# Performance work log

Hardware: AMD Instinct MI355X
Metric: run time of the kernel (lower is better)

The kernel has to match this reference:

```python
import jax, jax.numpy as jnp
import numpy as np


def setup_inputs() -> dict:
    key = jax.random.key(0)
    k1, k2 = jax.random.split(key)
    pred_pts = jax.random.normal(k1, (8, 3, 4096), dtype=jnp.float32)  # [B,3,N]
    gt_pts = jax.random.normal(k2, (8, 4096, 3), dtype=jnp.float32)    # [B,M,3]
    return {"pred_pts": pred_pts, "gt_pts": gt_pts}


def _chamfer(p, g):
    # p: [B,N,3], g: [B,M,3]
    # squared euclidean distance matrix via ||p||^2 + ||g||^2 - 2 p.g
    pn = jnp.sum(p * p, axis=-1)  # [B,N]
    gn = jnp.sum(g * g, axis=-1)  # [B,M]
    cross = jnp.einsum("bnd,bmd->bnm", p, g)  # [B,N,M]
    D = pn[:, :, None] + gn[:, None, :] - 2.0 * cross  # [B,N,M]
    dist1 = jnp.min(D, axis=2)  # [B,N] min over gt for each pred point
    dist2 = jnp.min(D, axis=1)  # [B,M] min over pred for each gt point
    return dist1, dist2


def reference(pred_pts, gt_pts):
    p = jnp.swapaxes(pred_pts, -2, -1).astype(jnp.float32)  # [B,N,3]
    g = gt_pts  # [B,M,3]
    dist1, dist2 = _chamfer(p, g)
    per_batch = jnp.mean(dist1, axis=1) + jnp.mean(dist2, axis=1)  # [B]
    loss = jnp.sum(per_batch) / gt_pts.shape[0]
    return loss
```

## Files before the change

kernel.cpp:

```cpp
#include <hip/hip_runtime.h>

#define NPTS 4096
#define BATCH 8
#define BLK 256
#define P 4
#define CHUNK 256
#define REPS 2
#define NSLOT 8
#define OWN_PER_BLK (BLK * P)
#define OWN_BLKS (NPTS / OWN_PER_BLK)
#define BLOCKS_PER_PASS (BATCH * OWN_BLKS * NSLOT)
#define TOTAL_BLOCKS (2 * BLOCKS_PER_PASS)
#define HALF_OWN (BATCH * NPTS)
#define TOTAL_OWN (2 * HALF_OWN)
#define COMBINE_BLOCKS (TOTAL_OWN / BLK)

__global__ __launch_bounds__(BLK, 2) void chamfer_partial_kernel(
    const float* __restrict__ pred,
    const float* __restrict__ gt,
    float* __restrict__ partial)
{
    __shared__ float4 s[CHUNK];

    const int bid  = blockIdx.x;
    const int pass = bid / BLOCKS_PER_PASS;
    int r = bid - pass * BLOCKS_PER_PASS;
    const int c = r % NSLOT;
    r /= NSLOT;
    const int b = r / OWN_BLKS;
    const int j = r - b * OWN_BLKS;
    const int t = threadIdx.x;

    const float* p = pred + (size_t)b * 3 * NPTS;
    const float* g = gt   + (size_t)b * NPTS * 3;

    float x[P], y[P], z[P];
    #pragma unroll
    for (int k = 0; k < P; ++k) {
        int idx = j * OWN_PER_BLK + k * BLK + t;
        if (pass == 0) { x[k] = p[idx]; y[k] = p[NPTS + idx]; z[k] = p[2 * NPTS + idx]; }
        else           { x[k] = g[idx * 3 + 0]; y[k] = g[idx * 3 + 1]; z[k] = g[idx * 3 + 2]; }
    }

    float qx, qy, qz;
    {
        int i = (c * REPS) * CHUNK + t;
        if (pass == 0) { qx = g[i * 3 + 0]; qy = g[i * 3 + 1]; qz = g[i * 3 + 2]; }
        else           { qx = p[i]; qy = p[NPTS + i]; qz = p[2 * NPTS + i]; }
    }

    float acc[P];
    #pragma unroll
    for (int k = 0; k < P; ++k) acc[k] = 3.4e38f;

    #pragma unroll
    for (int rep = 0; rep < REPS; ++rep) {
        __syncthreads();
        s[t] = make_float4(-2.f * qx, -2.f * qy, -2.f * qz,
                           fmaf(qx, qx, fmaf(qy, qy, qz * qz)));
        __syncthreads();

        if (rep + 1 < REPS) {
            int i = (c * REPS + rep + 1) * CHUNK + t;
            if (pass == 0) { qx = g[i * 3 + 0]; qy = g[i * 3 + 1]; qz = g[i * 3 + 2]; }
            else           { qx = p[i]; qy = p[NPTS + i]; qz = p[2 * NPTS + i]; }
        }

        #pragma unroll 2
        for (int ss = 0; ss < CHUNK; ss += 2) {
            float4 q0 = s[ss + 0];
            float4 q1 = s[ss + 1];
            #pragma unroll
            for (int k = 0; k < P; ++k) {
                float d0 = fmaf(x[k], q0.x, fmaf(y[k], q0.y, fmaf(z[k], q0.z, q0.w)));
                float d1 = fmaf(x[k], q1.x, fmaf(y[k], q1.y, fmaf(z[k], q1.z, q1.w)));
                acc[k] = fminf(fminf(d0, d1), acc[k]);
            }
        }
    }

    #pragma unroll
    for (int k = 0; k < P; ++k) {
        int idx = j * OWN_PER_BLK + k * BLK + t;
        int o = pass * HALF_OWN + b * NPTS + idx;
        float n2 = fmaf(x[k], x[k], fmaf(y[k], y[k], z[k] * z[k]));
        partial[(size_t)c * TOTAL_OWN + o] = n2 + acc[k];
    }
}

__global__ __launch_bounds__(BLK) void chamfer_combine_kernel(
    const float* __restrict__ partial, float* __restrict__ bsum)
{
    __shared__ float red[BLK / 64];
    const int t = threadIdx.x;
    const int o = blockIdx.x * BLK + t;
    float v = 3.4e38f;
    #pragma unroll
    for (int cc = 0; cc < NSLOT; ++cc)
        v = fminf(v, partial[(size_t)cc * TOTAL_OWN + o]);
    #pragma unroll
    for (int off = 32; off > 0; off >>= 1)
        v += __shfl_down(v, off, 64);
    if ((t & 63) == 0) red[t >> 6] = v;
    __syncthreads();
    if (t == 0) bsum[blockIdx.x] = red[0] + red[1] + red[2] + red[3];
}

__global__ __launch_bounds__(COMBINE_BLOCKS) void chamfer_final_kernel(
    const float* __restrict__ bsum, float* __restrict__ out)
{
    __shared__ float red[COMBINE_BLOCKS / 64];
    const int t = threadIdx.x;
    float v = bsum[t];
    #pragma unroll
    for (int off = 32; off > 0; off >>= 1)
        v += __shfl_down(v, off, 64);
    if ((t & 63) == 0) red[t >> 6] = v;
    __syncthreads();
    if (t == 0) {
        float s = 0.f;
        #pragma unroll
        for (int w = 0; w < COMBINE_BLOCKS / 64; ++w) s += red[w];
        out[0] = s * (1.0f / ((float)NPTS * (float)BATCH));
    }
}

extern "C" void kernel_launch(void* const* d_in, const int* in_sizes, int n_in,
                              void* d_out, int out_size, void* d_ws, size_t ws_size,
                              hipStream_t stream) {
    const float* pred = (const float*)d_in[0];
    const float* gt   = (const float*)d_in[1];
    float* out = (float*)d_out;

    float* partial = (float*)d_ws;
    float* bsum    = partial + (size_t)NSLOT * TOTAL_OWN;

    chamfer_partial_kernel<<<TOTAL_BLOCKS, BLK, 0, stream>>>(pred, gt, partial);
    chamfer_combine_kernel<<<COMBINE_BLOCKS, BLK, 0, stream>>>(partial, bsum);
    chamfer_final_kernel<<<1, COMBINE_BLOCKS, 0, stream>>>(bsum, out);
}
```

Measured before the change: 32.62 us.

## Use packed FP32 FMA with paired-query SoA shared layout and larger register tile

The inner distance loop now uses v_pk_fma_f32 to evaluate two query points per instruction. Query data is stored in shared memory in an interleaved pair layout. Each thread now owns 8 points instead of 4. The query set is split into 16 slots of one chunk each, replacing 8 slots of two chunks, so there is one shared-memory fill and no second barrier. The aim is to halve FMA issue count and cut LDS reads per FMA, at the cost of more registers, duplicated own-point vectors and a partial buffer twice as large for the combine kernel to read.

```diff
diff --git a/kernel.cpp b/kernel.cpp
--- a/kernel.cpp
+++ b/kernel.cpp
@@ -1,12 +1,13 @@
 #include <hip/hip_runtime.h>
+
+typedef float f32x2 __attribute__((ext_vector_type(2)));
 
 #define NPTS 4096
 #define BATCH 8
 #define BLK 256
-#define P 4
+#define P 8
 #define CHUNK 256
-#define REPS 2
-#define NSLOT 8
+#define NSLOT 16
 #define OWN_PER_BLK (BLK * P)
 #define OWN_BLKS (NPTS / OWN_PER_BLK)
 #define BLOCKS_PER_PASS (BATCH * OWN_BLKS * NSLOT)
@@ -15,12 +16,18 @@
 #define TOTAL_OWN (2 * HALF_OWN)
 #define COMBINE_BLOCKS (TOTAL_OWN / BLK)
 
+static __device__ __forceinline__ f32x2 pkfma(f32x2 a, f32x2 b, f32x2 c) {
+    f32x2 d;
+    asm("v_pk_fma_f32 %0, %1, %2, %3" : "=v"(d) : "v"(a), "v"(b), "v"(c));
+    return d;
+}
+
 __global__ __launch_bounds__(BLK, 2) void chamfer_partial_kernel(
     const float* __restrict__ pred,
     const float* __restrict__ gt,
     float* __restrict__ partial)
 {
-    __shared__ float4 s[CHUNK];
+    __shared__ float4 s4[2 * (CHUNK / 2)];
 
     const int bid  = blockIdx.x;
     const int pass = bid / BLOCKS_PER_PASS;
@@ -34,48 +41,51 @@
     const float* p = pred + (size_t)b * 3 * NPTS;
     const float* g = gt   + (size_t)b * NPTS * 3;
 
-    float x[P], y[P], z[P];
+    {
+        float qx, qy, qz;
+        int i = c * CHUNK + t;
+        if (pass == 0) { qx = g[i * 3 + 0]; qy = g[i * 3 + 1]; qz = g[i * 3 + 2]; }
+        else           { qx = p[i]; qy = p[NPTS + i]; qz = p[2 * NPTS + i]; }
+        float w = fmaf(qx, qx, fmaf(qy, qy, qz * qz));
+        float* sf = (float*)s4;
+        int base = (t >> 1) * 8, h = t & 1;
+        sf[base + 0 + h] = -2.f * qx;
+        sf[base + 2 + h] = -2.f * qy;
+        sf[base + 4 + h] = -2.f * qz;
+        sf[base + 6 + h] = w;
+    }
+
+    f32x2 X2[P], Y2[P], Z2[P];
+    float n2[P];
     #pragma unroll
     for (int k = 0; k < P; ++k) {
         int idx = j * OWN_PER_BLK + k * BLK + t;
-        if (pass == 0) { x[k] = p[idx]; y[k] = p[NPTS + idx]; z[k] = p[2 * NPTS + idx]; }
-        else           { x[k] = g[idx * 3 + 0]; y[k] = g[idx * 3 + 1]; z[k] = g[idx * 3 + 2]; }
+        float x, y, z;
+        if (pass == 0) { x = p[idx]; y = p[NPTS + idx]; z = p[2 * NPTS + idx]; }
+        else           { x = g[idx * 3 + 0]; y = g[idx * 3 + 1]; z = g[idx * 3 + 2]; }
+        X2[k].x = x; X2[k].y = x;
+        Y2[k].x = y; Y2[k].y = y;
+        Z2[k].x = z; Z2[k].y = z;
+        n2[k] = fmaf(x, x, fmaf(y, y, z * z));
     }
-
-    float qx, qy, qz;
-    {
-        int i = (c * REPS) * CHUNK + t;
-        if (pass == 0) { qx = g[i * 3 + 0]; qy = g[i * 3 + 1]; qz = g[i * 3 + 2]; }
-        else           { qx = p[i]; qy = p[NPTS + i]; qz = p[2 * NPTS + i]; }
-    }
+    __syncthreads();
 
     float acc[P];
     #pragma unroll
     for (int k = 0; k < P; ++k) acc[k] = 3.4e38f;
 
-    #pragma unroll
-    for (int rep = 0; rep < REPS; ++rep) {
-        __syncthreads();
-        s[t] = make_float4(-2.f * qx, -2.f * qy, -2.f * qz,
-                           fmaf(qx, qx, fmaf(qy, qy, qz * qz)));
-        __syncthreads();
-
-        if (rep + 1 < REPS) {
-            int i = (c * REPS + rep + 1) * CHUNK + t;
-            if (pass == 0) { qx = g[i * 3 + 0]; qy = g[i * 3 + 1]; qz = g[i * 3 + 2]; }
-            else           { qx = p[i]; qy = p[NPTS + i]; qz = p[2 * NPTS + i]; }
-        }
-
-        #pragma unroll 2
-        for (int ss = 0; ss < CHUNK; ss += 2) {
-            float4 q0 = s[ss + 0];
-            float4 q1 = s[ss + 1];
-            #pragma unroll
-            for (int k = 0; k < P; ++k) {
-                float d0 = fmaf(x[k], q0.x, fmaf(y[k], q0.y, fmaf(z[k], q0.z, q0.w)));
-                float d1 = fmaf(x[k], q1.x, fmaf(y[k], q1.y, fmaf(z[k], q1.z, q1.w)));
-                acc[k] = fminf(fminf(d0, d1), acc[k]);
-            }
+    #pragma unroll 4
+    for (int i = 0; i < CHUNK / 2; ++i) {
+        float4 h0 = s4[2 * i + 0];
+        float4 h1 = s4[2 * i + 1];
+        f32x2 xx; xx.x = h0.x; xx.y = h0.y;
+        f32x2 yy; yy.x = h0.z; yy.y = h0.w;
+        f32x2 zz; zz.x = h1.x; zz.y = h1.y;
+        f32x2 ww; ww.x = h1.z; ww.y = h1.w;
+        #pragma unroll
+        for (int k = 0; k < P; ++k) {
+            f32x2 d = pkfma(xx, X2[k], pkfma(yy, Y2[k], pkfma(zz, Z2[k], ww)));
+            acc[k] = fminf(fminf(d.x, d.y), acc[k]);
         }
     }
 
@@ -83,8 +93,7 @@
     for (int k = 0; k < P; ++k) {
         int idx = j * OWN_PER_BLK + k * BLK + t;
         int o = pass * HALF_OWN + b * NPTS + idx;
-        float n2 = fmaf(x[k], x[k], fmaf(y[k], y[k], z[k] * z[k]));
-        partial[(size_t)c * TOTAL_OWN + o] = n2 + acc[k];
+        partial[(size_t)c * TOTAL_OWN + o] = n2[k] + acc[k];
     }
 }
 
```

After: 32.88 us. About the same (+0.8%).
